# Optimization experiments

Hardware: AMD Instinct MI355X
Metric: run time of the kernel (lower is better)

The kernel has to match this reference:

```python
import jax, jax.numpy as jnp
import numpy as np

NEG_SLOPE = 0.2  # PyG GATConv default LeakyReLU slope


def gat_conv(x, src, dst, edge_attr, W, att_s, att_d, We, att_e, b, num_nodes):
    """PyG GATConv with heads=1, add_self_loops=False, edge_dim features."""
    h = x @ W                       # [N, d] shared lin for src/dst
    a_src = h @ att_s               # [N]
    a_dst = h @ att_d               # [N]
    a_edge = (edge_attr @ We) @ att_e  # [E]
    logits = jax.nn.leaky_relu(a_src[src] + a_dst[dst] + a_edge, NEG_SLOPE)  # [E]
    # segment softmax over edges sharing the same destination node
    seg_max = jax.ops.segment_max(logits, dst, num_segments=num_nodes)
    seg_max = jnp.where(jnp.isfinite(seg_max), seg_max, 0.0)
    num = jnp.exp(logits - seg_max[dst])
    den = jax.ops.segment_sum(num, dst, num_segments=num_nodes)
    alpha = num / (den[dst] + 1e-16)  # [E]
    out = jax.ops.segment_sum(alpha[:, None] * h[src], dst, num_segments=num_nodes)
    return out + b


def setup_inputs() -> dict:
    N, E, D = 50000, 800000, 64
    key = jax.random.key(0)
    ks = jax.random.split(key, 16)
    s = 1.0 / np.sqrt(D)
    inp = {
        "x": jax.random.normal(ks[0], (N, D), jnp.float32),
        "edge_index": jax.random.randint(ks[1], (2, E), 0, N, jnp.int32).astype(jnp.int64),
        "edge_attr": jax.random.uniform(ks[2], (E, 1), jnp.float32),
        # layer 1 params
        "W1": jax.random.normal(ks[3], (D, D), jnp.float32) * s,
        "att_s1": jax.random.normal(ks[4], (D,), jnp.float32) * s,
        "att_d1": jax.random.normal(ks[5], (D,), jnp.float32) * s,
        "We1": jax.random.normal(ks[6], (1, D), jnp.float32) * s,
        "att_e1": jax.random.normal(ks[7], (D,), jnp.float32) * s,
        "b1": jnp.zeros((D,), jnp.float32),
        # layer 2 params
        "W2": jax.random.normal(ks[8], (D, D), jnp.float32) * s,
        "att_s2": jax.random.normal(ks[9], (D,), jnp.float32) * s,
        "att_d2": jax.random.normal(ks[10], (D,), jnp.float32) * s,
        "We2": jax.random.normal(ks[11], (1, D), jnp.float32) * s,
        "att_e2": jax.random.normal(ks[12], (D,), jnp.float32) * s,
        "b2": jnp.zeros((D,), jnp.float32),
    }
    return inp


def reference(x, edge_index, edge_attr, W1, att_s1, att_d1, We1, att_e1, b1,
              W2, att_s2, att_d2, We2, att_e2, b2):
    N = x.shape[0]
    src, dst = edge_index[0], edge_index[1]
    h = gat_conv(x, src, dst, edge_attr, W1, att_s1, att_d1, We1, att_e1, b1, N)
    h = jax.nn.relu(h)  # dropout is identity in eval mode
    out = gat_conv(h, src, dst, edge_attr, W2, att_s2, att_d2, We2, att_e2, b2, N)
    return out
```

## Files before the change

### kernel.cpp

```cpp
#include <hip/hip_runtime.h>
#include <hip/hip_fp16.h>
#include <cstdint>

#define FEAT 64
#define NEG_SLOPE 0.2f
#define PBLK 128
#define NODE_SH 8
#define CAP 5120

__global__ void zero_prep_kernel(int* __restrict__ gcur,
                                 const float* __restrict__ We1, const float* __restrict__ ae1,
                                 const float* __restrict__ We2, const float* __restrict__ ae2,
                                 float* __restrict__ cbuf) {
    int tid = threadIdx.x;
    if (tid < 64) {
        for (int i = tid; i < 256; i += 64) gcur[i] = 0;
    } else if (tid < 192) {
        int lane = tid & 63;
        bool second = tid >= 128;
        const float* a = second ? We2 : We1;
        const float* b = second ? ae2 : ae1;
        float v = a[lane] * b[lane];
        #pragma unroll
        for (int off = 32; off; off >>= 1) v += __shfl_xor(v, off, 64);
        if (lane == 0) cbuf[second ? 1 : 0] = v;
    }
}

__global__ __launch_bounds__(256) void coarse_gemm1_kernel(
        const int* __restrict__ src, const int* __restrict__ dst,
        const float* __restrict__ eattr, int* __restrict__ gcur,
        int2* __restrict__ tmp, int E,
        const float* __restrict__ X, const float* __restrict__ W,
        const float* __restrict__ att_s, const float* __restrict__ att_d,
        __half* __restrict__ Hh, float* __restrict__ a_src,
        float* __restrict__ a_dst, int N) {
    __shared__ float smem[FEAT * FEAT];
    int tid = threadIdx.x;

    if (blockIdx.x < PBLK) {
        int* lcnt = (int*)smem;
        int* lcur = (int*)smem + 256;
        int p = blockIdx.x;
        lcnt[tid] = 0;
        __syncthreads();
        int ch = (E + PBLK - 1) / PBLK;
        int beg = p * ch, end = min(E, beg + ch);
        for (int e = beg + tid; e < end; e += 256)
            atomicAdd(&lcnt[dst[e] >> NODE_SH], 1);
        __syncthreads();
        int c = lcnt[tid];
        lcur[tid] = c ? atomicAdd(&gcur[tid], c) : 0;
        __syncthreads();
        for (int e = beg + tid; e < end; e += 256) {
            int d = dst[e];
            int bkt = d >> NODE_SH;
            int slot = atomicAdd(&lcur[bkt], 1);
            tmp[(size_t)bkt * CAP + slot] =
                make_int2((int)(((unsigned)d << 16) | (unsigned)src[e]),
                          __float_as_int(eattr[e]));
        }
        return;
    }

    int wave = tid >> 6, lane = tid & 63;
    const float4* W4 = (const float4*)W;
    float4* Ws4 = (float4*)smem;
    #pragma unroll
    for (int i = 0; i < 4; ++i) Ws4[tid + i * 256] = W4[tid + i * 256];

    int row0 = (blockIdx.x - PBLK) * 32 + wave * 8;
    float xv[8];
    #pragma unroll
    for (int r = 0; r < 8; ++r) {
        int row = row0 + r;
        xv[r] = (row < N) ? X[(size_t)row * FEAT + lane] : 0.f;
    }
    __syncthreads();

    float acc[8] = {0.f, 0.f, 0.f, 0.f, 0.f, 0.f, 0.f, 0.f};
    #pragma unroll
    for (int k = 0; k < FEAT; ++k) {
        float wk = smem[k * FEAT + lane];
        #pragma unroll
        for (int r = 0; r < 8; ++r) {
            float xk = __uint_as_float(__builtin_amdgcn_readlane(__float_as_uint(xv[r]), k));
            acc[r] = fmaf(xk, wk, acc[r]);
        }
    }

    float as_w = att_s[lane], ad_w = att_d[lane];
    #pragma unroll
    for (int r = 0; r < 8; ++r) {
        int row = row0 + r;
        if (row >= N) break;
        Hh[(size_t)row * FEAT + lane] = __float2half(acc[r]);
        float sv = acc[r] * as_w;
        float dv = acc[r] * ad_w;
        #pragma unroll
        for (int off = 32; off; off >>= 1) {
            sv += __shfl_xor(sv, off, 64);
            dv += __shfl_xor(dv, off, 64);
        }
        if (lane == 0) { a_src[row] = sv; a_dst[row] = dv; }
    }
}

__global__ __launch_bounds__(256) void fine_kernel(
        const int2* __restrict__ tmp, const int* __restrict__ gcur,
        int2* __restrict__ rowptr2, unsigned* __restrict__ epack, int N) {
    __shared__ int cnt[256];
    __shared__ int wsum[4];
    int b = blockIdx.x, tid = threadIdx.x;
    int base = b * CAP;
    int cb = gcur[b];
    cnt[tid] = 0;
    __syncthreads();
    for (int i = tid; i < cb; i += 256)
        atomicAdd(&cnt[((unsigned)tmp[base + i].x >> 16) & 255], 1);
    __syncthreads();
    int lane = tid & 63, wave = tid >> 6;
    int v = cnt[tid], orig = v;
    #pragma unroll
    for (int off = 1; off < 64; off <<= 1) {
        int t = __shfl_up(v, off, 64);
        if (lane >= off) v += t;
    }
    if (lane == 63) wsum[wave] = v;
    __syncthreads();
    int add = 0;
    for (int w = 0; w < wave; ++w) add += wsum[w];
    int excl = base + v + add - orig;
    int node = (b << NODE_SH) + tid;
    if (node < N) rowptr2[node] = make_int2(excl, excl + orig);
    __syncthreads();
    cnt[tid] = excl;
    __syncthreads();
    for (int i = tid; i < cb; i += 256) {
        int2 t2 = tmp[base + i];
        int d8 = ((unsigned)t2.x >> 16) & 255;
        int pos = atomicAdd(&cnt[d8], 1);
        unsigned packed = ((unsigned)t2.x << 16) |
                          (unsigned)__half_as_ushort(__float2half(__int_as_float(t2.y)));
        epack[pos] = packed;
    }
}

__global__ __launch_bounds__(256) void gemm2_att_kernel(
        const __half* __restrict__ Xh, const float* __restrict__ W,
        const float* __restrict__ att_s, const float* __restrict__ att_d,
        __half* __restrict__ Hh, float* __restrict__ a_src,
        float* __restrict__ a_dst, int N) {
    __shared__ float Ws[FEAT * FEAT];
    int tid = threadIdx.x, wave = tid >> 6, lane = tid & 63;

    const float4* W4 = (const float4*)W;
    float4* Ws4 = (float4*)Ws;
    #pragma unroll
    for (int i = 0; i < 4; ++i) Ws4[tid + i * 256] = W4[tid + i * 256];

    int row0 = blockIdx.x * 32 + wave * 8;
    float xv[8];
    #pragma unroll
    for (int r = 0; r < 8; ++r) {
        int row = row0 + r;
        xv[r] = (row < N) ? __half2float(Xh[(size_t)row * FEAT + lane]) : 0.f;
    }
    __syncthreads();

    float acc[8] = {0.f, 0.f, 0.f, 0.f, 0.f, 0.f, 0.f, 0.f};
    #pragma unroll
    for (int k = 0; k < FEAT; ++k) {
        float wk = Ws[k * FEAT + lane];
        #pragma unroll
        for (int r = 0; r < 8; ++r) {
            float xk = __uint_as_float(__builtin_amdgcn_readlane(__float_as_uint(xv[r]), k));
            acc[r] = fmaf(xk, wk, acc[r]);
        }
    }

    float as_w = att_s[lane], ad_w = att_d[lane];
    #pragma unroll
    for (int r = 0; r < 8; ++r) {
        int row = row0 + r;
        if (row >= N) break;
        Hh[(size_t)row * FEAT + lane] = __float2half(acc[r]);
        float sv = acc[r] * as_w;
        float dv = acc[r] * ad_w;
        #pragma unroll
        for (int off = 32; off; off >>= 1) {
            sv += __shfl_xor(sv, off, 64);
            dv += __shfl_xor(dv, off, 64);
        }
        if (lane == 0) { a_src[row] = sv; a_dst[row] = dv; }
    }
}

template <bool FINAL>
__global__ __launch_bounds__(256) void fused_agg_kernel(
        const int2* __restrict__ rowptr2, const unsigned* __restrict__ epack,
        const float* __restrict__ a_src, const float* __restrict__ a_dst,
        const float* __restrict__ cptr, const uint2* __restrict__ Hh2,
        const float* __restrict__ bias, void* __restrict__ OUTv, int N) {
    int tid = threadIdx.x;
    int wave = tid >> 6, lane = tid & 63;
    int grp = lane >> 4, gl = lane & 15;
    int grpBase = grp << 4;
    int node = blockIdx.x * 16 + wave * 4 + grp;
    bool valid = node < N;
    int2 be = valid ? rowptr2[node] : make_int2(0, 0);
    int beg = be.x, end = be.y;
    float c = *cptr;
    float adn = valid ? a_dst[node] : 0.f;

    float den = 0.f;
    float4 a0 = {0,0,0,0}, a1 = {0,0,0,0}, a2 = {0,0,0,0}, a3 = {0,0,0,0};

    int nchunk = (end - beg + 15) >> 4;
    int wc = nchunk;
    wc = max(wc, __shfl_xor(wc, 16, 64));
    wc = max(wc, __shfl_xor(wc, 32, 64));

    for (int ch = 0; ch < wc; ++ch) {
        int j = beg + ch * 16 + gl;
        int s = 0;
        float w = 0.f;
        if (j < end) {
            unsigned ep = epack[j];
            s = (int)(ep >> 16);
            float ea = __half2float(__ushort_as_half((unsigned short)(ep & 0xffffu)));
            float l = fmaf(c, ea, a_src[s] + adn);
            l = (l > 0.f) ? l : NEG_SLOPE * l;
            w = __expf(l);
        }
        den += w;

        #pragma unroll
        for (int half = 0; half < 2; ++half) {
            int kb = grpBase + half * 8;
            int   s0 = __shfl(s, kb + 0, 64), s1 = __shfl(s, kb + 1, 64);
            int   s2 = __shfl(s, kb + 2, 64), s3 = __shfl(s, kb + 3, 64);
            int   s4 = __shfl(s, kb + 4, 64), s5 = __shfl(s, kb + 5, 64);
            int   s6 = __shfl(s, kb + 6, 64), s7 = __shfl(s, kb + 7, 64);
            float w0 = __shfl(w, kb + 0, 64), w1 = __shfl(w, kb + 1, 64);
            float w2 = __shfl(w, kb + 2, 64), w3 = __shfl(w, kb + 3, 64);
            float w4 = __shfl(w, kb + 4, 64), w5 = __shfl(w, kb + 5, 64);
            float w6 = __shfl(w, kb + 6, 64), w7 = __shfl(w, kb + 7, 64);
            uint2 u0 = Hh2[(size_t)s0 * 16 + gl];
            uint2 u1 = Hh2[(size_t)s1 * 16 + gl];
            uint2 u2 = Hh2[(size_t)s2 * 16 + gl];
            uint2 u3 = Hh2[(size_t)s3 * 16 + gl];
            uint2 u4 = Hh2[(size_t)s4 * 16 + gl];
            uint2 u5 = Hh2[(size_t)s5 * 16 + gl];
            uint2 u6 = Hh2[(size_t)s6 * 16 + gl];
            uint2 u7 = Hh2[(size_t)s7 * 16 + gl];
            float2 f00 = __half22float2(*(__half2*)&u0.x), f01 = __half22float2(*(__half2*)&u0.y);
            float2 f10 = __half22float2(*(__half2*)&u1.x), f11 = __half22float2(*(__half2*)&u1.y);
            float2 f20 = __half22float2(*(__half2*)&u2.x), f21 = __half22float2(*(__half2*)&u2.y);
            float2 f30 = __half22float2(*(__half2*)&u3.x), f31 = __half22float2(*(__half2*)&u3.y);
            float2 f40 = __half22float2(*(__half2*)&u4.x), f41 = __half22float2(*(__half2*)&u4.y);
            float2 f50 = __half22float2(*(__half2*)&u5.x), f51 = __half22float2(*(__half2*)&u5.y);
            float2 f60 = __half22float2(*(__half2*)&u6.x), f61 = __half22float2(*(__half2*)&u6.y);
            float2 f70 = __half22float2(*(__half2*)&u7.x), f71 = __half22float2(*(__half2*)&u7.y);
            a0.x = fmaf(w0, f00.x, a0.x); a0.y = fmaf(w0, f00.y, a0.y);
            a0.z = fmaf(w0, f01.x, a0.z); a0.w = fmaf(w0, f01.y, a0.w);
            a1.x = fmaf(w1, f10.x, a1.x); a1.y = fmaf(w1, f10.y, a1.y);
            a1.z = fmaf(w1, f11.x, a1.z); a1.w = fmaf(w1, f11.y, a1.w);
            a2.x = fmaf(w2, f20.x, a2.x); a2.y = fmaf(w2, f20.y, a2.y);
            a2.z = fmaf(w2, f21.x, a2.z); a2.w = fmaf(w2, f21.y, a2.w);
            a3.x = fmaf(w3, f30.x, a3.x); a3.y = fmaf(w3, f30.y, a3.y);
            a3.z = fmaf(w3, f31.x, a3.z); a3.w = fmaf(w3, f31.y, a3.w);
            a0.x = fmaf(w4, f40.x, a0.x); a0.y = fmaf(w4, f40.y, a0.y);
            a0.z = fmaf(w4, f41.x, a0.z); a0.w = fmaf(w4, f41.y, a0.w);
            a1.x = fmaf(w5, f50.x, a1.x); a1.y = fmaf(w5, f50.y, a1.y);
            a1.z = fmaf(w5, f51.x, a1.z); a1.w = fmaf(w5, f51.y, a1.w);
            a2.x = fmaf(w6, f60.x, a2.x); a2.y = fmaf(w6, f60.y, a2.y);
            a2.z = fmaf(w6, f61.x, a2.z); a2.w = fmaf(w6, f61.y, a2.w);
            a3.x = fmaf(w7, f70.x, a3.x); a3.y = fmaf(w7, f70.y, a3.y);
            a3.z = fmaf(w7, f71.x, a3.z); a3.w = fmaf(w7, f71.y, a3.w);
        }
    }

    den += __shfl_xor(den, 1, 64);
    den += __shfl_xor(den, 2, 64);
    den += __shfl_xor(den, 4, 64);
    den += __shfl_xor(den, 8, 64);

    if (valid) {
        float4 b4 = ((const float4*)bias)[gl];
        float inv = 1.f / (den + 1e-16f);
        float ox = (a0.x + a1.x + a2.x + a3.x) * inv + b4.x;
        float oy = (a0.y + a1.y + a2.y + a3.y) * inv + b4.y;
        float oz = (a0.z + a1.z + a2.z + a3.z) * inv + b4.z;
        float ow = (a0.w + a1.w + a2.w + a3.w) * inv + b4.w;
        if constexpr (FINAL) {
            ((float4*)OUTv)[(size_t)node * 16 + gl] = make_float4(ox, oy, oz, ow);
        } else {
            __half2 h01 = __floats2half2_rn(fmaxf(ox, 0.f), fmaxf(oy, 0.f));
            __half2 h23 = __floats2half2_rn(fmaxf(oz, 0.f), fmaxf(ow, 0.f));
            uint2 u;
            u.x = *(unsigned*)&h01;
            u.y = *(unsigned*)&h23;
            ((uint2*)OUTv)[(size_t)node * 16 + gl] = u;
        }
    }
}


static inline size_t align256(size_t x) { return (x + 255) & ~size_t(255); }

extern "C" void kernel_launch(void* const* d_in, const int* in_sizes, int n_in,
                              void* d_out, int out_size, void* d_ws, size_t ws_size,
                              hipStream_t stream) {
    const float* x        = (const float*)d_in[0];
    const int*   eidx     = (const int*)d_in[1];
    const float* eattr    = (const float*)d_in[2];
    const float* W1       = (const float*)d_in[3];
    const float* att_s1   = (const float*)d_in[4];
    const float* att_d1   = (const float*)d_in[5];
    const float* We1      = (const float*)d_in[6];
    const float* att_e1   = (const float*)d_in[7];
    const float* b1       = (const float*)d_in[8];
    const float* W2       = (const float*)d_in[9];
    const float* att_s2   = (const float*)d_in[10];
    const float* att_d2   = (const float*)d_in[11];
    const float* We2      = (const float*)d_in[12];
    const float* att_e2   = (const float*)d_in[13];
    const float* b2       = (const float*)d_in[14];
    float* OUT = (float*)d_out;

    const int N = in_sizes[0] / FEAT;
    const int E = in_sizes[2];
    const int* src = eidx;
    const int* dst = eidx + E;
    const int NB = (N + (1 << NODE_SH) - 1) >> NODE_SH;

    char* ws = (char*)d_ws;
    size_t off = 0;
    __half* Hh     = (__half*)(ws + off); off = align256(off + (size_t)N * FEAT * 2);
    __half* out1h  = (__half*)(ws + off); off = align256(off + (size_t)N * FEAT * 2);
    float* a_src   = (float*)(ws + off); off = align256(off + (size_t)N * 4);
    float* a_dst   = (float*)(ws + off); off = align256(off + (size_t)N * 4);
    int2*  rowptr2 = (int2*)(ws + off); off = align256(off + (size_t)N * 8);
    int2*  tmp     = (int2*)(ws + off); off = align256(off + (size_t)NB * CAP * 8);
    unsigned* epack= (unsigned*)(ws + off); off = align256(off + (size_t)NB * CAP * 4);
    int*   gcur    = (int*)(ws + off); off = align256(off + 256 * 4);
    float* cbuf    = (float*)(ws + off); off = align256(off + 2 * 4);
    (void)ws_size;

    const int gemmBlocks = (N + 31) / 32;
    const int aggBlocks  = (N + 15) / 16;

    zero_prep_kernel<<<1, 256, 0, stream>>>(gcur, We1, att_e1, We2, att_e2, cbuf);

    coarse_gemm1_kernel<<<PBLK + gemmBlocks, 256, 0, stream>>>(
        src, dst, eattr, gcur, tmp, E,
        x, W1, att_s1, att_d1, Hh, a_src, a_dst, N);

    fine_kernel<<<NB, 256, 0, stream>>>(tmp, gcur, rowptr2, epack, N);

    fused_agg_kernel<false><<<aggBlocks, 256, 0, stream>>>(rowptr2, epack, a_src, a_dst,
                                                           cbuf + 0, (const uint2*)Hh, b1,
                                                           out1h, N);

    gemm2_att_kernel<<<gemmBlocks, 256, 0, stream>>>(out1h, W2, att_s2, att_d2,
                                                     Hh, a_src, a_dst, N);
    fused_agg_kernel<true><<<aggBlocks, 256, 0, stream>>>(rowptr2, epack, a_src, a_dst,
                                                          cbuf + 1, (const uint2*)Hh, b2,
                                                          OUT, N);
}
```

Baseline: 134.0 us.

## Sort nodes by degree per block and skip empty half-chunks in aggregation

The fine CSR kernel now builds a per-block histogram of node in-degrees and writes a degree-sorted node permutation. The aggregation kernels read nodes through this permutation, so the four 16-lane groups in a wave get similar degrees and wave-level loop counts diverge less. The aggregation also skips the second 8-edge half of a chunk when no group in the wave has more than 8 remaining edges. This costs an extra indirection load per node and scattered output writes, and padded nodes past N now get rowptr entries written.

```diff
diff --git a/kernel.cpp b/kernel.cpp
--- a/kernel.cpp
+++ b/kernel.cpp
@@ -108,19 +108,24 @@
 
 __global__ __launch_bounds__(256) void fine_kernel(
         const int2* __restrict__ tmp, const int* __restrict__ gcur,
-        int2* __restrict__ rowptr2, unsigned* __restrict__ epack, int N) {
+        int2* __restrict__ rowptr2, unsigned* __restrict__ epack,
+        int* __restrict__ nodeperm, int N) {
     __shared__ int cnt[256];
     __shared__ int wsum[4];
+    __shared__ int hist[64];
+    __shared__ int hcur[64];
     int b = blockIdx.x, tid = threadIdx.x;
     int base = b * CAP;
     int cb = gcur[b];
     cnt[tid] = 0;
+    if (tid < 64) hist[tid] = 0;
     __syncthreads();
     for (int i = tid; i < cb; i += 256)
         atomicAdd(&cnt[((unsigned)tmp[base + i].x >> 16) & 255], 1);
     __syncthreads();
     int lane = tid & 63, wave = tid >> 6;
-    int v = cnt[tid], orig = v;
+    int deg = cnt[tid];
+    int v = deg;
     #pragma unroll
     for (int off = 1; off < 64; off <<= 1) {
         int t = __shfl_up(v, off, 64);
@@ -130,12 +135,25 @@
     __syncthreads();
     int add = 0;
     for (int w = 0; w < wave; ++w) add += wsum[w];
-    int excl = base + v + add - orig;
+    int excl = base + v + add - deg;
     int node = (b << NODE_SH) + tid;
-    if (node < N) rowptr2[node] = make_int2(excl, excl + orig);
-    __syncthreads();
+    rowptr2[node] = make_int2(excl, excl + deg);
+    int key = min(deg, 63);
+    atomicAdd(&hist[key], 1);
+    __syncthreads();
+    if (tid < 64) {
+        int h = hist[tid], s = h;
+        #pragma unroll
+        for (int off = 1; off < 64; off <<= 1) {
+            int t = __shfl_up(s, off, 64);
+            if (tid >= off) s += t;
+        }
+        hcur[tid] = s - h;
+    }
     cnt[tid] = excl;
     __syncthreads();
+    int sortpos = atomicAdd(&hcur[key], 1);
+    nodeperm[(b << NODE_SH) + sortpos] = node;
     for (int i = tid; i < cb; i += 256) {
         int2 t2 = tmp[base + i];
         int d8 = ((unsigned)t2.x >> 16) & 255;
@@ -199,6 +217,7 @@
 template <bool FINAL>
 __global__ __launch_bounds__(256) void fused_agg_kernel(
         const int2* __restrict__ rowptr2, const unsigned* __restrict__ epack,
+        const int* __restrict__ nodeperm,
         const float* __restrict__ a_src, const float* __restrict__ a_dst,
         const float* __restrict__ cptr, const uint2* __restrict__ Hh2,
         const float* __restrict__ bias, void* __restrict__ OUTv, int N) {
@@ -206,10 +225,11 @@
     int wave = tid >> 6, lane = tid & 63;
     int grp = lane >> 4, gl = lane & 15;
     int grpBase = grp << 4;
-    int node = blockIdx.x * 16 + wave * 4 + grp;
+    int slot = blockIdx.x * 16 + wave * 4 + grp;
+    int node = nodeperm[slot];
+    int2 be = rowptr2[node];
+    int beg = be.x, end = be.y;
     bool valid = node < N;
-    int2 be = valid ? rowptr2[node] : make_int2(0, 0);
-    int beg = be.x, end = be.y;
     float c = *cptr;
     float adn = valid ? a_dst[node] : 0.f;
 
@@ -235,8 +255,15 @@
         }
         den += w;
 
+        int rem = end - (beg + ch * 16);
+        rem = min(max(rem, 0), 16);
+        int mrem = rem;
+        mrem = max(mrem, __shfl_xor(mrem, 16, 64));
+        mrem = max(mrem, __shfl_xor(mrem, 32, 64));
+
         #pragma unroll
         for (int half = 0; half < 2; ++half) {
+            if (half == 1 && mrem <= 8) break;
             int kb = grpBase + half * 8;
             int   s0 = __shfl(s, kb + 0, 64), s1 = __shfl(s, kb + 1, 64);
             int   s2 = __shfl(s, kb + 2, 64), s3 = __shfl(s, kb + 3, 64);
@@ -334,6 +361,7 @@
     const int* src = eidx;
     const int* dst = eidx + E;
     const int NB = (N + (1 << NODE_SH) - 1) >> NODE_SH;
+    const int NPAD = NB << NODE_SH;
 
     char* ws = (char*)d_ws;
     size_t off = 0;
@@ -341,7 +369,8 @@
     __half* out1h  = (__half*)(ws + off); off = align256(off + (size_t)N * FEAT * 2);
     float* a_src   = (float*)(ws + off); off = align256(off + (size_t)N * 4);
     float* a_dst   = (float*)(ws + off); off = align256(off + (size_t)N * 4);
-    int2*  rowptr2 = (int2*)(ws + off); off = align256(off + (size_t)N * 8);
+    int2*  rowptr2 = (int2*)(ws + off); off = align256(off + (size_t)NPAD * 8);
+    int*   nodeperm= (int*)(ws + off); off = align256(off + (size_t)NPAD * 4);
     int2*  tmp     = (int2*)(ws + off); off = align256(off + (size_t)NB * CAP * 8);
     unsigned* epack= (unsigned*)(ws + off); off = align256(off + (size_t)NB * CAP * 4);
     int*   gcur    = (int*)(ws + off); off = align256(off + 256 * 4);
@@ -349,7 +378,7 @@
     (void)ws_size;
 
     const int gemmBlocks = (N + 31) / 32;
-    const int aggBlocks  = (N + 15) / 16;
+    const int aggBlocks  = NPAD / 16;
 
     zero_prep_kernel<<<1, 256, 0, stream>>>(gcur, We1, att_e1, We2, att_e2, cbuf);
 
@@ -357,15 +386,15 @@
         src, dst, eattr, gcur, tmp, E,
         x, W1, att_s1, att_d1, Hh, a_src, a_dst, N);
 
-    fine_kernel<<<NB, 256, 0, stream>>>(tmp, gcur, rowptr2, epack, N);
-
-    fused_agg_kernel<false><<<aggBlocks, 256, 0, stream>>>(rowptr2, epack, a_src, a_dst,
-                                                           cbuf + 0, (const uint2*)Hh, b1,
-                                                           out1h, N);
+    fine_kernel<<<NB, 256, 0, stream>>>(tmp, gcur, rowptr2, epack, nodeperm, N);
+
+    fused_agg_kernel<false><<<aggBlocks, 256, 0, stream>>>(rowptr2, epack, nodeperm,
+                                                           a_src, a_dst, cbuf + 0,
+                                                           (const uint2*)Hh, b1, out1h, N);
 
     gemm2_att_kernel<<<gemmBlocks, 256, 0, stream>>>(out1h, W2, att_s2, att_d2,
                                                      Hh, a_src, a_dst, N);
-    fused_agg_kernel<true><<<aggBlocks, 256, 0, stream>>>(rowptr2, epack, a_src, a_dst,
-                                                          cbuf + 1, (const uint2*)Hh, b2,
-                                                          OUT, N);
-}
+    fused_agg_kernel<true><<<aggBlocks, 256, 0, stream>>>(rowptr2, epack, nodeperm,
+                                                          a_src, a_dst, cbuf + 1,
+                                                          (const uint2*)Hh, b2, OUT, N);
+}
```

After: 140.4 us. +4.7%, slower.
